# Kernel optimization log

Measured on AMD Instinct MI355X. Metric: run time of the kernel, lower is better.

The kernel has to match this reference:

```python
import jax, jax.numpy as jnp
import numpy as np

DECAY = 0.8
COMMITMENT_WEIGHT = 1.0
EPS = 1e-5


def setup_inputs() -> dict:
    key = jax.random.key(0)
    k1, k2, k3 = jax.random.split(key, 3)
    B, T, D, K = 16, 2048, 512, 8192
    x = jax.random.normal(k1, (B, T, D), dtype=jnp.float32)
    embed = jax.random.normal(k2, (D, K), dtype=jnp.float32)
    cluster_size = jnp.ones((K,), dtype=jnp.float32)
    embed_avg = jax.random.normal(k3, (D, K), dtype=jnp.float32)
    return {"x": x, "embed": embed, "cluster_size": cluster_size, "embed_avg": embed_avg}


def reference(x, embed, cluster_size, embed_avg):
    B, T, D = x.shape
    K = embed.shape[1]
    flat = x.reshape(-1, D)  # [N, D]

    # squared L2 distance to each code: ||f||^2 - 2 f.e + ||e||^2  -> [N, K]
    dist = (flat * flat).sum(-1, keepdims=True) \
        - 2.0 * (flat @ embed) \
        + (embed * embed).sum(0, keepdims=True)
    embed_ind = jnp.argmin(dist, axis=1)  # [N] (== argmax of -dist)

    quantize = jnp.take(embed.T, embed_ind, axis=0).reshape(B, T, D)

    # ---- EMA codebook statistics (training-mode buffer updates) ----
    onehot_sum = jnp.zeros((K,), dtype=flat.dtype).at[embed_ind].add(1.0)  # [K]
    # flat.T @ onehot == segment-sum of tokens per code, transposed -> [D, K]
    embed_sum = jax.ops.segment_sum(flat, embed_ind, num_segments=K).T
    new_cluster_size = cluster_size * DECAY + (1.0 - DECAY) * onehot_sum
    new_embed_avg = embed_avg * DECAY + (1.0 - DECAY) * embed_sum
    n = new_cluster_size.sum()
    cs = (new_cluster_size + EPS) / (n + K * EPS) * n
    new_embed = new_embed_avg / cs[None, :]
    # (random re-init of unused codes is omitted: non-deterministic side effect)

    commitment_loss = jnp.mean((jax.lax.stop_gradient(quantize) - x) ** 2) * COMMITMENT_WEIGHT
    quantize_st = x + jax.lax.stop_gradient(quantize - x)  # straight-through

    return (quantize_st, embed_ind.reshape(B, T), commitment_loss,
            new_embed, new_cluster_size, new_embed_avg)
```

## Files before the change

### kernel.cpp

```cpp
#include <hip/hip_runtime.h>

#define NTOK   32768
#define DDIM   512
#define KCODES 8192
#define DK     (DDIM * KCODES)
#define DECAYF 0.8f
#define EPSF   1e-5f

using short8 = __attribute__((ext_vector_type(8))) short;
using f32x4  = __attribute__((ext_vector_type(4))) float;

#define WS_ESUMT   0
#define WS_ONEHOT  DK
#define WS_ENORM   (DK + 8192)
#define WS_SCAL    (DK + 16384)
#define WS_PART    (DK + 16400)
#define WS_EMBEDT  (WS_PART + 2 * NTOK)
#define WS_EHI     (WS_EMBEDT + DK)
#define WS_ELO     (WS_EHI + DK / 2)
#define WS_ZERO_BYTES ((size_t)(DK + 16400) * 4)

__device__ __forceinline__ unsigned short bf16rne(float f) {
  unsigned u = __float_as_uint(f);
  unsigned r = u + 0x7FFFu + ((u >> 16) & 1u);
  return (unsigned short)(r >> 16);
}

__device__ __forceinline__ void gload_lds16(const unsigned short* g, unsigned short* l) {
  __builtin_amdgcn_global_load_lds(
      (const __attribute__((address_space(1))) unsigned int*)g,
      (__attribute__((address_space(3))) unsigned int*)l, 16, 0, 0);
}

__global__ __launch_bounds__(256) void split_x_kernel(
    const float* __restrict__ x, unsigned short* __restrict__ hi,
    unsigned short* __restrict__ lo) {
  const size_t i = ((size_t)blockIdx.x * 256 + threadIdx.x) * 8;
  const float4 v0 = *(const float4*)&x[i];
  const float4 v1 = *(const float4*)&x[i + 4];
  const float v[8] = {v0.x, v0.y, v0.z, v0.w, v1.x, v1.y, v1.z, v1.w};
  unsigned short h[8], l[8];
#pragma unroll
  for (int j = 0; j < 8; ++j) {
    h[j] = bf16rne(v[j]);
    l[j] = bf16rne(v[j] - __uint_as_float((unsigned)h[j] << 16));
  }
  uint4 H, L;
  H.x = h[0] | ((unsigned)h[1] << 16); H.y = h[2] | ((unsigned)h[3] << 16);
  H.z = h[4] | ((unsigned)h[5] << 16); H.w = h[6] | ((unsigned)h[7] << 16);
  L.x = l[0] | ((unsigned)l[1] << 16); L.y = l[2] | ((unsigned)l[3] << 16);
  L.z = l[4] | ((unsigned)l[5] << 16); L.w = l[6] | ((unsigned)l[7] << 16);
  *(uint4*)&hi[i] = H;
  *(uint4*)&lo[i] = L;
}

__global__ __launch_bounds__(256) void transpose_split_kernel(
    const float* __restrict__ embed, float* __restrict__ embedT,
    unsigned short* __restrict__ ehi, unsigned short* __restrict__ elo,
    float* __restrict__ e_norm) {
  __shared__ float tile[32][33];
  __shared__ float part[8][32];
  const int k0 = blockIdx.x * 32;
  const int d0 = blockIdx.y * 32;
  const int tx = threadIdx.x;
  const int ty = threadIdx.y;
  float sq = 0.f;
#pragma unroll
  for (int j = 0; j < 4; ++j) {
    const int dl = ty + j * 8;
    const float v = embed[(size_t)(d0 + dl) * KCODES + k0 + tx];
    tile[dl][tx] = v;
    sq += v * v;
  }
  part[ty][tx] = sq;
  __syncthreads();
  if (ty == 0) {
    float s = 0.f;
#pragma unroll
    for (int j = 0; j < 8; ++j) s += part[j][tx];
    atomicAdd(&e_norm[k0 + tx], s);
  }
#pragma unroll
  for (int j = 0; j < 4; ++j) {
    const int kl = ty + j * 8;
    const size_t idx = (size_t)(k0 + kl) * DDIM + d0 + tx;
    const float v = tile[tx][kl];
    embedT[idx] = v;
    const unsigned short h = bf16rne(v);
    ehi[idx] = h;
    elo[idx] = bf16rne(v - __uint_as_float((unsigned)h << 16));
  }
}

__global__ __launch_bounds__(256) void argmin_mfma_kernel(
    const unsigned short* __restrict__ xhi, const unsigned short* __restrict__ xlo,
    const unsigned short* __restrict__ ehi, const unsigned short* __restrict__ elo,
    const float* __restrict__ e_norm, unsigned long long* __restrict__ partials) {
  __shared__ unsigned short Ahs[128 * 32];
  __shared__ unsigned short Als[128 * 32];
  __shared__ unsigned short Bhs[128 * 32];
  __shared__ unsigned short Bls[128 * 32];

  const int t    = threadIdx.x;
  const int wid  = t >> 6;
  const int lid  = t & 63;
  const int kblk = blockIdx.x;
  const int tokbase = blockIdx.y * 128;
  const int kbase   = kblk * 128;

  const int wrow = wid >> 1, wcol = wid & 1;
  const int m16  = lid & 15, kq = lid >> 4;

  const int srow = lid >> 2;
  const int gcol = ((lid & 3) ^ ((srow >> 1) & 3)) * 8;

  const int fsw = (kq ^ ((m16 >> 1) & 3)) * 8;

  f32x4 acc[4][4];
#pragma unroll
  for (int i = 0; i < 4; ++i)
#pragma unroll
    for (int j = 0; j < 4; ++j) acc[i][j] = (f32x4)0.f;

  const unsigned short* Ahg = xhi + (size_t)tokbase * DDIM;
  const unsigned short* Alg = xlo + (size_t)tokbase * DDIM;
  const unsigned short* Bhg = ehi + (size_t)kbase * DDIM;
  const unsigned short* Blg = elo + (size_t)kbase * DDIM;

#pragma unroll 1
  for (int d0 = 0; d0 < DDIM; d0 += 32) {
    __syncthreads();
#pragma unroll
    for (int p = 0; p < 2; ++p) {
      const int chunk = wid + p * 4;
      const size_t go = (size_t)(chunk * 16 + srow) * DDIM + d0 + gcol;
      gload_lds16(Ahg + go, &Ahs[chunk * 512]);
      gload_lds16(Alg + go, &Als[chunk * 512]);
      gload_lds16(Bhg + go, &Bhs[chunk * 512]);
      gload_lds16(Blg + go, &Bls[chunk * 512]);
    }
    __syncthreads();
    short8 bh[4], bl[4];
#pragma unroll
    for (int j = 0; j < 4; ++j) {
      const int r = (wcol * 64 + j * 16 + m16) * 32 + fsw;
      bh[j] = *(const short8*)&Bhs[r];
      bl[j] = *(const short8*)&Bls[r];
    }
#pragma unroll
    for (int i = 0; i < 4; ++i) {
      const int r = (wrow * 64 + i * 16 + m16) * 32 + fsw;
      const short8 ah = *(const short8*)&Ahs[r];
      const short8 al = *(const short8*)&Als[r];
#pragma unroll
      for (int j = 0; j < 4; ++j) {
        acc[i][j] = __builtin_amdgcn_mfma_f32_16x16x32_bf16(ah, bh[j], acc[i][j], 0, 0, 0);
        acc[i][j] = __builtin_amdgcn_mfma_f32_16x16x32_bf16(ah, bl[j], acc[i][j], 0, 0, 0);
        acc[i][j] = __builtin_amdgcn_mfma_f32_16x16x32_bf16(al, bh[j], acc[i][j], 0, 0, 0);
      }
    }
  }

  float en[4];
#pragma unroll
  for (int j = 0; j < 4; ++j)
    en[j] = e_norm[kbase + wcol * 64 + j * 16 + m16];

  __syncthreads();
  unsigned long long* red = (unsigned long long*)Ahs;
#pragma unroll
  for (int i = 0; i < 4; ++i) {
#pragma unroll
    for (int r = 0; r < 4; ++r) {
      unsigned long long best = 0xFFFFFFFFFFFFFFFFull;
#pragma unroll
      for (int j = 0; j < 4; ++j) {
        const float s = en[j] - 2.0f * acc[i][j][r];
        unsigned u = __float_as_uint(s);
        u = (u & 0x80000000u) ? ~u : (u | 0x80000000u);
        const unsigned k = (unsigned)(kbase + wcol * 64 + j * 16 + m16);
        const unsigned long long c = ((unsigned long long)u << 32) | k;
        best = (c < best) ? c : best;
      }
#pragma unroll
      for (int s = 1; s < 16; s <<= 1) {
        const unsigned long long c = __shfl_xor(best, s);
        best = (c < best) ? c : best;
      }
      if (m16 == 0)
        red[(wrow * 64 + i * 16 + kq * 4 + r) * 2 + wcol] = best;
    }
  }
  __syncthreads();
  if (t < 128) {
    const unsigned long long a0 = red[t * 2], a1 = red[t * 2 + 1];
    const unsigned long long m = (a0 < a1) ? a0 : a1;
    atomicMin(&partials[tokbase + t], m);
  }
}

__global__ __launch_bounds__(128) void gather_stats_kernel(
    const float* __restrict__ x, const float* __restrict__ embedT,
    const unsigned long long* __restrict__ partials,
    float* __restrict__ quant_out, float* __restrict__ indf_out,
    float* __restrict__ embed_sumT, float* __restrict__ onehot,
    float* __restrict__ scal) {
  const int n = blockIdx.x;
  __shared__ int s_ind;
  __shared__ float wsum[2];
  if (threadIdx.x == 0) {
    const int k = (int)(partials[n] & 0xFFFFFFFFull);
    s_ind = k;
    indf_out[n] = (float)k;
    atomicAdd(&onehot[k], 1.0f);
  }
  __syncthreads();
  const int k = s_ind;
  const int d4 = threadIdx.x * 4;
  const float4 e  = *(const float4*)&embedT[(size_t)k * DDIM + d4];
  const float4 xv = *(const float4*)&x[(size_t)n * DDIM + d4];
  *(float4*)&quant_out[(size_t)n * DDIM + d4] = e;
  atomicAdd(&embed_sumT[(size_t)k * DDIM + d4 + 0], xv.x);
  atomicAdd(&embed_sumT[(size_t)k * DDIM + d4 + 1], xv.y);
  atomicAdd(&embed_sumT[(size_t)k * DDIM + d4 + 2], xv.z);
  atomicAdd(&embed_sumT[(size_t)k * DDIM + d4 + 3], xv.w);
  const float dx0 = e.x - xv.x, dx1 = e.y - xv.y, dx2 = e.z - xv.z, dx3 = e.w - xv.w;
  float ls = dx0 * dx0 + dx1 * dx1 + dx2 * dx2 + dx3 * dx3;
#pragma unroll
  for (int off = 32; off > 0; off >>= 1) ls += __shfl_down(ls, off);
  if ((threadIdx.x & 63) == 0) wsum[threadIdx.x >> 6] = ls;
  __syncthreads();
  if (threadIdx.x == 0) atomicAdd(&scal[0], wsum[0] + wsum[1]);
}

__global__ __launch_bounds__(256) void cluster_kernel(
    const float* __restrict__ cluster_size, const float* __restrict__ onehot,
    float* __restrict__ ncs_out, float* __restrict__ scal) {
  const int k = blockIdx.x * 256 + threadIdx.x;
  const float v = cluster_size[k] * DECAYF + (1.0f - DECAYF) * onehot[k];
  ncs_out[k] = v;
  float s = v;
#pragma unroll
  for (int off = 32; off > 0; off >>= 1) s += __shfl_down(s, off);
  __shared__ float w[4];
  if ((threadIdx.x & 63) == 0) w[threadIdx.x >> 6] = s;
  __syncthreads();
  if (threadIdx.x == 0) atomicAdd(&scal[1], w[0] + w[1] + w[2] + w[3]);
}

__global__ __launch_bounds__(256) void finalize_kernel(
    const float* __restrict__ embed_avg, const float* __restrict__ embed_sumT,
    const float* __restrict__ ncs, const float* __restrict__ scal,
    float* __restrict__ out_embed, float* __restrict__ out_avg,
    float* __restrict__ out_loss) {
  const int idx = blockIdx.x * 256 + threadIdx.x;
  const int d = idx >> 13;
  const int k = idx & (KCODES - 1);
  const float ea = embed_avg[idx];
  const float es = embed_sumT[(size_t)k * DDIM + d];
  const float nea = DECAYF * ea + (1.0f - DECAYF) * es;
  out_avg[idx] = nea;
  const float nsum = scal[1];
  const float cs = (ncs[k] + EPSF) / (nsum + (float)KCODES * EPSF) * nsum;
  out_embed[idx] = nea / cs;
  if (idx == 0) out_loss[0] = scal[0] * (1.0f / ((float)NTOK * (float)DDIM));
}

extern "C" void kernel_launch(void* const* d_in, const int* in_sizes, int n_in,
                              void* d_out, int out_size, void* d_ws, size_t ws_size,
                              hipStream_t stream) {
  (void)in_sizes; (void)n_in; (void)out_size; (void)ws_size;
  const float* x            = (const float*)d_in[0];
  const float* embed        = (const float*)d_in[1];
  const float* cluster_size = (const float*)d_in[2];
  const float* embed_avg    = (const float*)d_in[3];

  float* out = (float*)d_out;
  float* out_quant = out;
  float* out_indf  = out + 16777216;
  float* out_loss  = out + 16777216 + 32768;
  float* out_embed = out + 16777216 + 32768 + 1;
  float* out_ncs   = out_embed + DK;
  float* out_avg   = out_ncs + KCODES;

  float* ws = (float*)d_ws;
  float* esumT  = ws + WS_ESUMT;
  float* onehot = ws + WS_ONEHOT;
  float* e_norm = ws + WS_ENORM;
  float* scal   = ws + WS_SCAL;
  unsigned long long* partials = (unsigned long long*)(ws + WS_PART);
  float* embedT = ws + WS_EMBEDT;
  unsigned short* ehi = (unsigned short*)(ws + WS_EHI);
  unsigned short* elo = (unsigned short*)(ws + WS_ELO);

  unsigned short* xhi = (unsigned short*)d_out;
  unsigned short* xlo = xhi + (size_t)NTOK * DDIM;

  hipMemsetAsync(d_ws, 0, WS_ZERO_BYTES, stream);
  hipMemsetAsync((char*)d_ws + (size_t)WS_PART * 4, 0xFF, (size_t)NTOK * 8, stream);

  split_x_kernel<<<NTOK * DDIM / 8 / 256, 256, 0, stream>>>(x, xhi, xlo);
  transpose_split_kernel<<<dim3(KCODES / 32, DDIM / 32), dim3(32, 8), 0, stream>>>(
      embed, embedT, ehi, elo, e_norm);

  argmin_mfma_kernel<<<dim3(64, 256), 256, 0, stream>>>(
      xhi, xlo, ehi, elo, e_norm, partials);

  gather_stats_kernel<<<NTOK, 128, 0, stream>>>(
      x, embedT, partials, out_quant, out_indf, esumT, onehot, scal);

  cluster_kernel<<<KCODES / 256, 256, 0, stream>>>(cluster_size, onehot, out_ncs, scal);

  finalize_kernel<<<DK / 256, 256, 0, stream>>>(
      embed_avg, esumT, out_ncs, scal, out_embed, out_avg, out_loss);
}
```

Measured before the change: 1.576 ms.

## Replace atomic segment-sum with counting-sort gather and tiled transposed finalize

```diff
diff --git a/kernel.cpp b/kernel.cpp
--- a/kernel.cpp
+++ b/kernel.cpp
@@ -10,15 +10,19 @@
 using short8 = __attribute__((ext_vector_type(8))) short;
 using f32x4  = __attribute__((ext_vector_type(4))) float;
 
-#define WS_ESUMT   0
-#define WS_ONEHOT  DK
-#define WS_ENORM   (DK + 8192)
-#define WS_SCAL    (DK + 16384)
-#define WS_PART    (DK + 16400)
-#define WS_EMBEDT  (WS_PART + 2 * NTOK)
+#define WS_ONEHOT  0
+#define WS_ENORM   KCODES
+#define WS_SCAL    (2 * KCODES)
+#define WS_CURSOR  (2 * KCODES + 16)
+#define WS_ZERO_BYTES ((size_t)(3 * KCODES + 16) * 4)
+#define WS_PART    (3 * KCODES + 16)
+#define WS_IND     (WS_PART + 2 * NTOK)
+#define WS_OFF     (WS_IND + NTOK)
+#define WS_SORT    (WS_OFF + KCODES)
+#define WS_ESUMT   (WS_SORT + NTOK)
+#define WS_EMBEDT  (WS_ESUMT + DK)
 #define WS_EHI     (WS_EMBEDT + DK)
 #define WS_ELO     (WS_EHI + DK / 2)
-#define WS_ZERO_BYTES ((size_t)(DK + 16400) * 4)
 
 __device__ __forceinline__ unsigned short bf16rne(float f) {
   unsigned u = __float_as_uint(f);
@@ -92,7 +96,7 @@
   }
 }
 
-__global__ __launch_bounds__(256) void argmin_mfma_kernel(
+__global__ __launch_bounds__(256, 3) void argmin_mfma_kernel(
     const unsigned short* __restrict__ xhi, const unsigned short* __restrict__ xlo,
     const unsigned short* __restrict__ ehi, const unsigned short* __restrict__ elo,
     const float* __restrict__ e_norm, unsigned long long* __restrict__ partials) {
@@ -113,8 +117,7 @@
 
   const int srow = lid >> 2;
   const int gcol = ((lid & 3) ^ ((srow >> 1) & 3)) * 8;
-
-  const int fsw = (kq ^ ((m16 >> 1) & 3)) * 8;
+  const int fsw  = (kq ^ ((m16 >> 1) & 3)) * 8;
 
   f32x4 acc[4][4];
 #pragma unroll
@@ -199,31 +202,94 @@
   }
 }
 
-__global__ __launch_bounds__(128) void gather_stats_kernel(
+__global__ __launch_bounds__(256) void argmin_finish_kernel(
+    const unsigned long long* __restrict__ partials, int* __restrict__ ind,
+    float* __restrict__ indf_out, float* __restrict__ onehot) {
+  const int n = blockIdx.x * 256 + threadIdx.x;
+  const int k = (int)(partials[n] & 0xFFFFFFFFull);
+  ind[n] = k;
+  indf_out[n] = (float)k;
+  atomicAdd(&onehot[k], 1.0f);
+}
+
+__global__ __launch_bounds__(256) void scan_cluster_kernel(
+    const float* __restrict__ onehot, const float* __restrict__ cluster_size,
+    int* __restrict__ code_offset, float* __restrict__ ncs_out,
+    float* __restrict__ scal) {
+  const int t = threadIdx.x;
+  __shared__ int ssum[256];
+  __shared__ float fsum[256];
+  int cnt[32];
+  int local = 0;
+  float ncs_sum = 0.f;
+#pragma unroll
+  for (int c = 0; c < 32; ++c) {
+    const int k = t * 32 + c;
+    cnt[c] = (int)onehot[k];
+    local += cnt[c];
+    const float v = cluster_size[k] * DECAYF + (1.0f - DECAYF) * onehot[k];
+    ncs_out[k] = v;
+    ncs_sum += v;
+  }
+  ssum[t] = local;
+  fsum[t] = ncs_sum;
+  __syncthreads();
+  for (int off = 1; off < 256; off <<= 1) {
+    const int v = (t >= off) ? ssum[t - off] : 0;
+    __syncthreads();
+    ssum[t] += v;
+    __syncthreads();
+  }
+  int running = ssum[t] - local;
+#pragma unroll
+  for (int c = 0; c < 32; ++c) {
+    code_offset[t * 32 + c] = running;
+    running += cnt[c];
+  }
+  for (int off = 128; off > 0; off >>= 1) {
+    __syncthreads();
+    if (t < off) fsum[t] += fsum[t + off];
+  }
+  if (t == 0) scal[1] = fsum[0];
+}
+
+__global__ __launch_bounds__(256) void scatter_kernel(
+    const int* __restrict__ ind, const int* __restrict__ code_offset,
+    int* __restrict__ cursor, int* __restrict__ sorted) {
+  const int n = blockIdx.x * 256 + threadIdx.x;
+  const int k = ind[n];
+  const int pos = code_offset[k] + atomicAdd(&cursor[k], 1);
+  sorted[pos] = n;
+}
+
+__global__ __launch_bounds__(128) void segsum_kernel(
+    const float* __restrict__ x, const int* __restrict__ sorted,
+    const int* __restrict__ code_offset, const float* __restrict__ onehot,
+    float* __restrict__ esumT) {
+  const int k = blockIdx.x;
+  const int off = code_offset[k];
+  const int cnt = (int)onehot[k];
+  const int d4 = threadIdx.x * 4;
+  float4 acc = {0.f, 0.f, 0.f, 0.f};
+  for (int tk = 0; tk < cnt; ++tk) {
+    const int n = sorted[off + tk];
+    const float4 v = *(const float4*)&x[(size_t)n * DDIM + d4];
+    acc.x += v.x; acc.y += v.y; acc.z += v.z; acc.w += v.w;
+  }
+  *(float4*)&esumT[(size_t)k * DDIM + d4] = acc;
+}
+
+__global__ __launch_bounds__(128) void quantize_loss_kernel(
     const float* __restrict__ x, const float* __restrict__ embedT,
-    const unsigned long long* __restrict__ partials,
-    float* __restrict__ quant_out, float* __restrict__ indf_out,
-    float* __restrict__ embed_sumT, float* __restrict__ onehot,
+    const int* __restrict__ ind, float* __restrict__ quant_out,
     float* __restrict__ scal) {
   const int n = blockIdx.x;
-  __shared__ int s_ind;
+  const int k = ind[n];
   __shared__ float wsum[2];
-  if (threadIdx.x == 0) {
-    const int k = (int)(partials[n] & 0xFFFFFFFFull);
-    s_ind = k;
-    indf_out[n] = (float)k;
-    atomicAdd(&onehot[k], 1.0f);
-  }
-  __syncthreads();
-  const int k = s_ind;
   const int d4 = threadIdx.x * 4;
   const float4 e  = *(const float4*)&embedT[(size_t)k * DDIM + d4];
   const float4 xv = *(const float4*)&x[(size_t)n * DDIM + d4];
   *(float4*)&quant_out[(size_t)n * DDIM + d4] = e;
-  atomicAdd(&embed_sumT[(size_t)k * DDIM + d4 + 0], xv.x);
-  atomicAdd(&embed_sumT[(size_t)k * DDIM + d4 + 1], xv.y);
-  atomicAdd(&embed_sumT[(size_t)k * DDIM + d4 + 2], xv.z);
-  atomicAdd(&embed_sumT[(size_t)k * DDIM + d4 + 3], xv.w);
   const float dx0 = e.x - xv.x, dx1 = e.y - xv.y, dx2 = e.z - xv.z, dx3 = e.w - xv.w;
   float ls = dx0 * dx0 + dx1 * dx1 + dx2 * dx2 + dx3 * dx3;
 #pragma unroll
@@ -233,37 +299,36 @@
   if (threadIdx.x == 0) atomicAdd(&scal[0], wsum[0] + wsum[1]);
 }
 
-__global__ __launch_bounds__(256) void cluster_kernel(
-    const float* __restrict__ cluster_size, const float* __restrict__ onehot,
-    float* __restrict__ ncs_out, float* __restrict__ scal) {
-  const int k = blockIdx.x * 256 + threadIdx.x;
-  const float v = cluster_size[k] * DECAYF + (1.0f - DECAYF) * onehot[k];
-  ncs_out[k] = v;
-  float s = v;
-#pragma unroll
-  for (int off = 32; off > 0; off >>= 1) s += __shfl_down(s, off);
-  __shared__ float w[4];
-  if ((threadIdx.x & 63) == 0) w[threadIdx.x >> 6] = s;
-  __syncthreads();
-  if (threadIdx.x == 0) atomicAdd(&scal[1], w[0] + w[1] + w[2] + w[3]);
-}
-
 __global__ __launch_bounds__(256) void finalize_kernel(
-    const float* __restrict__ embed_avg, const float* __restrict__ embed_sumT,
+    const float* __restrict__ embed_avg, const float* __restrict__ esumT,
     const float* __restrict__ ncs, const float* __restrict__ scal,
     float* __restrict__ out_embed, float* __restrict__ out_avg,
     float* __restrict__ out_loss) {
-  const int idx = blockIdx.x * 256 + threadIdx.x;
-  const int d = idx >> 13;
-  const int k = idx & (KCODES - 1);
-  const float ea = embed_avg[idx];
-  const float es = embed_sumT[(size_t)k * DDIM + d];
-  const float nea = DECAYF * ea + (1.0f - DECAYF) * es;
-  out_avg[idx] = nea;
+  __shared__ float tile[32][33];
+  const int k0 = blockIdx.x * 32;
+  const int d0 = blockIdx.y * 32;
+  const int tx = threadIdx.x;
+  const int ty = threadIdx.y;
+#pragma unroll
+  for (int j = 0; j < 4; ++j) {
+    const int kl = ty + j * 8;
+    tile[kl][tx] = esumT[(size_t)(k0 + kl) * DDIM + d0 + tx];
+  }
   const float nsum = scal[1];
-  const float cs = (ncs[k] + EPSF) / (nsum + (float)KCODES * EPSF) * nsum;
-  out_embed[idx] = nea / cs;
-  if (idx == 0) out_loss[0] = scal[0] * (1.0f / ((float)NTOK * (float)DDIM));
+  const float cs = (ncs[k0 + tx] + EPSF) / (nsum + (float)KCODES * EPSF) * nsum;
+  const float inv_cs = 1.0f / cs;
+  __syncthreads();
+#pragma unroll
+  for (int j = 0; j < 4; ++j) {
+    const int dl = ty + j * 8;
+    const size_t idx = (size_t)(d0 + dl) * KCODES + k0 + tx;
+    const float ea = embed_avg[idx];
+    const float nea = DECAYF * ea + (1.0f - DECAYF) * tile[tx][dl];
+    out_avg[idx] = nea;
+    out_embed[idx] = nea * inv_cs;
+  }
+  if (blockIdx.x == 0 && blockIdx.y == 0 && tx == 0 && ty == 0)
+    out_loss[0] = scal[0] * (1.0f / ((float)NTOK * (float)DDIM));
 }
 
 extern "C" void kernel_launch(void* const* d_in, const int* in_sizes, int n_in,
@@ -284,11 +349,15 @@
   float* out_avg   = out_ncs + KCODES;
 
   float* ws = (float*)d_ws;
-  float* esumT  = ws + WS_ESUMT;
   float* onehot = ws + WS_ONEHOT;
   float* e_norm = ws + WS_ENORM;
   float* scal   = ws + WS_SCAL;
+  int*   cursor = (int*)(ws + WS_CURSOR);
   unsigned long long* partials = (unsigned long long*)(ws + WS_PART);
+  int*   ind    = (int*)(ws + WS_IND);
+  int*   coff   = (int*)(ws + WS_OFF);
+  int*   sorted = (int*)(ws + WS_SORT);
+  float* esumT  = ws + WS_ESUMT;
   float* embedT = ws + WS_EMBEDT;
   unsigned short* ehi = (unsigned short*)(ws + WS_EHI);
   unsigned short* elo = (unsigned short*)(ws + WS_ELO);
@@ -306,11 +375,12 @@
   argmin_mfma_kernel<<<dim3(64, 256), 256, 0, stream>>>(
       xhi, xlo, ehi, elo, e_norm, partials);
 
-  gather_stats_kernel<<<NTOK, 128, 0, stream>>>(
-      x, embedT, partials, out_quant, out_indf, esumT, onehot, scal);
-
-  cluster_kernel<<<KCODES / 256, 256, 0, stream>>>(cluster_size, onehot, out_ncs, scal);
-
-  finalize_kernel<<<DK / 256, 256, 0, stream>>>(
+  argmin_finish_kernel<<<NTOK / 256, 256, 0, stream>>>(partials, ind, out_indf, onehot);
+  scan_cluster_kernel<<<1, 256, 0, stream>>>(onehot, cluster_size, coff, out_ncs, scal);
+  scatter_kernel<<<NTOK / 256, 256, 0, stream>>>(ind, coff, cursor, sorted);
+  segsum_kernel<<<KCODES, 128, 0, stream>>>(x, sorted, coff, onehot, esumT);
+  quantize_loss_kernel<<<NTOK, 128, 0, stream>>>(x, embedT, ind, out_quant, scal);
+
+  finalize_kernel<<<dim3(KCODES / 32, DDIM / 32), dim3(32, 8), 0, stream>>>(
       embed_avg, esumT, out_ncs, scal, out_embed, out_avg, out_loss);
 }
```

After: 1.638 ms. +3.9%, slower.
